# Optimization experiments

Hardware: AMD Instinct MI355X
Metric: run time of the kernel (lower is better)

Reference implementation:

```python
import jax, jax.numpy as jnp
import numpy as np
from jax import lax

C = 16
FIRE_RATE = 0.5
STEP_SIZE = 1.0


def _fixed_kernel():
    _i = np.array([0, 1, 0], dtype=np.float32)
    I = np.outer(_i, _i)
    dx = (np.outer([1, 2, 1], [-1, 0, 1]) / 8.0).astype(np.float32)
    dy = dx.T
    lap = np.array([[0.25, 0.5, 0.25], [0.5, -3, 0.5], [0.25, 0.5, 0.25]], dtype=np.float32)
    av = np.ones((3, 3), dtype=np.float32) / 9.0
    k = np.stack([I, dx, dy, lap, av], -1)            # [3,3,5]
    k = np.tile(k, (1, 1, C))                          # [3,3,5*C], channel-major blocks of 5
    return jnp.asarray(k[:, :, None, :])               # HWIO [3,3,1,5*C]

KERNEL = _fixed_kernel()


def setup_inputs() -> dict:
    key = jax.random.key(0)
    ks = jax.random.split(key, 5)
    B, S = 4, 512
    x = jax.random.normal(ks[0], (B, S, S, C), jnp.float32)
    noise = jax.random.normal(ks[1], (B, S, S, 1), jnp.float32)
    W1 = jax.random.normal(ks[2], (5 * C, 4 * C), jnp.float32) * (1.0 / np.sqrt(5 * C))
    b1 = jnp.zeros((4 * C,), jnp.float32)
    W2 = jax.random.normal(ks[3], (4 * C, 2 * C), jnp.float32) * (1.0 / np.sqrt(4 * C))
    b2 = jnp.zeros((2 * C,), jnp.float32)
    W3 = jax.random.normal(ks[4], (2 * C, C), jnp.float32) * (1.0 / np.sqrt(2 * C))
    b3 = jnp.zeros((C,), jnp.float32)
    return {"x": x, "noise": noise, "W1": W1, "b1": b1, "W2": W2, "b2": b2, "W3": W3, "b3": b3}


def _swish(z):
    return z * jax.nn.sigmoid(z)


def reference(x, noise, W1, b1, W2, b2, W3, b3):
    # perceive: depthwise 3x3 conv with 5 fixed kernels per channel -> [B,H,W,5*C]
    y = lax.conv_general_dilated(
        x, KERNEL, window_strides=(1, 1), padding="SAME",
        dimension_numbers=("NHWC", "HWIO", "NHWC"), feature_group_count=C)
    # 3-layer 1x1 conv MLP
    h = _swish(jnp.einsum("bhwc,cd->bhwd", y, W1) + b1)
    h = _swish(jnp.einsum("bhwc,cd->bhwd", h, W2) + b2)
    dx = (jnp.einsum("bhwc,cd->bhwd", h, W3) + b3) * STEP_SIZE
    # stochastic update mask: normal noise <= fire_rate
    update_mask = (noise <= FIRE_RATE).astype(jnp.float32)  # [B,H,W,1]
    return x + dx * update_mask
```

## Files before the change

### kernel.cpp

```cpp
#include <hip/hip_runtime.h>

typedef __bf16 bf16x8 __attribute__((ext_vector_type(8)));
typedef float f32x16 __attribute__((ext_vector_type(16)));
typedef short short8 __attribute__((ext_vector_type(8)));

#define S 512
#define CH 16

#define ELT(v, c) ((c)==0 ? (v).x : (c)==1 ? (v).y : (c)==2 ? (v).z : (v).w)

__device__ __forceinline__ float swishf(float z) {
    return z * __builtin_amdgcn_rcpf(1.0f + __expf(-z));
}

__global__ void prep_weights(const float* __restrict__ W1, const float* __restrict__ b1,
                             const float* __restrict__ W2, const float* __restrict__ b2,
                             const float* __restrict__ W3, const float* __restrict__ b3,
                             short* __restrict__ wsf, float* __restrict__ wsb)
{
    int idx = blockIdx.x * 256 + threadIdx.x;
    if (idx < 12288) {
        int fi = idx >> 9, rem = idx & 511;
        int lane = rem >> 3, j = rem & 7;
        int col = lane & 31, hi = lane >> 5;
        int jp = (j & 3) + 8 * (j >> 2);
        float v;
        if (fi < 18) {
            int n = fi / 9, s = fi - n * 9;
            int dr = s / 3, dc = s - dr * 3;
            int c = hi * 8 + j;
            const float wgt0 = (dr == 1) ? 2.f : 1.f;
            const float wgt1 = (dc == 1) ? 2.f : 1.f;
            const float dlt0 = (float)(dr - 1);
            const float dlt1 = (float)(dc - 1);
            const float lapm[9] = {0.25f, 0.5f, 0.25f, 0.5f, -3.f, 0.5f, 0.25f, 0.5f, 0.25f};
            float kI  = (s == 4) ? 1.f : 0.f;
            float kdx = wgt0 * dlt1 * 0.125f;
            float kdy = dlt0 * wgt1 * 0.125f;
            float klp = lapm[s];
            float kav = 1.f / 9.f;
            const float* wr = W1 + (c * 5) * 64 + n * 32 + col;
            v = kI * wr[0] + kdx * wr[64] + kdy * wr[128] + klp * wr[192] + kav * wr[256];
        } else if (fi < 22) {
            int t = fi - 18;
            int rowW = (t >> 1) * 32 + 4 * hi + (t & 1) * 16 + jp;
            v = W2[rowW * 32 + col];
        } else {
            int t = fi - 22;
            int rowW = 4 * hi + t * 16 + jp;
            v = (col < 16) ? W3[rowW * 16 + col] : 0.0f;
        }
        __bf16 b = (__bf16)v;
        wsf[idx] = __builtin_bit_cast(short, b);
    }
    if (blockIdx.x == 0) {
        int t = threadIdx.x;
        if (t < 64) wsb[t] = b1[t];
        else if (t < 96) wsb[t] = b2[t - 64];
        else if (t < 112) wsb[t] = b3[t - 96];
    }
}

__global__ __launch_bounds__(256, 4) void nca_fused(
    const float* __restrict__ x, const float* __restrict__ noise,
    const short* __restrict__ wsf, const float* __restrict__ wsb,
    float* __restrict__ out)
{
    __shared__ short wlds[12288];
    {
        const int4* src = reinterpret_cast<const int4*>(wsf);
        int4* dst = reinterpret_cast<int4*>(wlds);
        for (int i = threadIdx.x; i < 1536; i += 256) dst[i] = src[i];
    }
    __syncthreads();

    const int tid = threadIdx.x;
    const int bid = blockIdx.x;
    const int st = bid & 15;
    const int rg = (bid >> 4) & 127;
    const int bb = bid >> 11;
    const int wv = tid >> 6, lane = tid & 63;
    const int col = lane & 31, hi = lane >> 5;
    const int row = rg * 4 + wv;
    const int px0 = st * 32;

    short8 bfr[9];
    {
        const float* xb = x + (size_t)bb * S * S * CH + hi * 8;
        const bool rowInt = (row > 0) && (row < S - 1);
        const bool colInt = (px0 != 0) && (px0 != 480);
        if (rowInt && colInt) {
#pragma unroll
            for (int dr = 0; dr < 3; ++dr) {
                const float* rp = xb + ((size_t)(row - 1 + dr) * S + (px0 + col - 1)) * CH;
#pragma unroll
                for (int dc = 0; dc < 3; ++dc) {
                    float4 v0 = *reinterpret_cast<const float4*>(rp + dc * CH);
                    float4 v1 = *reinterpret_cast<const float4*>(rp + dc * CH + 4);
                    short8 f;
                    f[0] = __builtin_bit_cast(short, (__bf16)v0.x);
                    f[1] = __builtin_bit_cast(short, (__bf16)v0.y);
                    f[2] = __builtin_bit_cast(short, (__bf16)v0.z);
                    f[3] = __builtin_bit_cast(short, (__bf16)v0.w);
                    f[4] = __builtin_bit_cast(short, (__bf16)v1.x);
                    f[5] = __builtin_bit_cast(short, (__bf16)v1.y);
                    f[6] = __builtin_bit_cast(short, (__bf16)v1.z);
                    f[7] = __builtin_bit_cast(short, (__bf16)v1.w);
                    bfr[dr * 3 + dc] = f;
                }
            }
        } else {
#pragma unroll
            for (int dr = 0; dr < 3; ++dr) {
                int gr = row - 1 + dr;
                bool rok = (unsigned)gr < (unsigned)S;
                int grc = min(max(gr, 0), S - 1);
#pragma unroll
                for (int dc = 0; dc < 3; ++dc) {
                    int c = px0 + col - 1 + dc;
                    bool ok = rok && ((unsigned)c < (unsigned)S);
                    int cl = min(max(c, 0), S - 1);
                    const float* p = xb + ((size_t)grc * S + cl) * CH;
                    float4 v0 = *reinterpret_cast<const float4*>(p);
                    float4 v1 = *reinterpret_cast<const float4*>(p + 4);
                    if (!ok) { v0 = make_float4(0.f,0.f,0.f,0.f); v1 = v0; }
                    short8 f;
                    f[0] = __builtin_bit_cast(short, (__bf16)v0.x);
                    f[1] = __builtin_bit_cast(short, (__bf16)v0.y);
                    f[2] = __builtin_bit_cast(short, (__bf16)v0.z);
                    f[3] = __builtin_bit_cast(short, (__bf16)v0.w);
                    f[4] = __builtin_bit_cast(short, (__bf16)v1.x);
                    f[5] = __builtin_bit_cast(short, (__bf16)v1.y);
                    f[6] = __builtin_bit_cast(short, (__bf16)v1.z);
                    f[7] = __builtin_bit_cast(short, (__bf16)v1.w);
                    bfr[dr * 3 + dc] = f;
                }
            }
        }
    }

    const short8* wf = reinterpret_cast<const short8*>(wlds);

    f32x16 acc1[2];
#pragma unroll
    for (int n = 0; n < 2; ++n) {
        f32x16 acc = {};
#pragma unroll
        for (int s = 0; s < 9; ++s) {
            bf16x8 a = __builtin_bit_cast(bf16x8, wf[(n * 9 + s) * 64 + lane]);
            acc = __builtin_amdgcn_mfma_f32_32x32x16_bf16(a, __builtin_bit_cast(bf16x8, bfr[s]), acc, 0, 0, 0);
        }
        acc1[n] = acc;
    }

    short8 b2f[4];
#pragma unroll
    for (int t = 0; t < 4; ++t) {
        int n = t >> 1;
        float4 bq0 = *reinterpret_cast<const float4*>(wsb + n * 32 + 4 * hi + 16 * (t & 1));
        float4 bq1 = *reinterpret_cast<const float4*>(wsb + n * 32 + 4 * hi + 16 * (t & 1) + 8);
#pragma unroll
        for (int j = 0; j < 8; ++j) {
            float bias = (j < 4) ? ELT(bq0, j & 3) : ELT(bq1, j & 3);
            float h = swishf(acc1[n][(t & 1) * 8 + j] + bias);
            b2f[t][j] = __builtin_bit_cast(short, (__bf16)h);
        }
    }

    f32x16 acc2 = {};
#pragma unroll
    for (int t = 0; t < 4; ++t) {
        bf16x8 a = __builtin_bit_cast(bf16x8, wf[(18 + t) * 64 + lane]);
        acc2 = __builtin_amdgcn_mfma_f32_32x32x16_bf16(a, __builtin_bit_cast(bf16x8, b2f[t]), acc2, 0, 0, 0);
    }

    short8 b3f[2];
#pragma unroll
    for (int t = 0; t < 2; ++t) {
        float4 cq0 = *reinterpret_cast<const float4*>(wsb + 64 + 4 * hi + 16 * t);
        float4 cq1 = *reinterpret_cast<const float4*>(wsb + 64 + 4 * hi + 16 * t + 8);
#pragma unroll
        for (int j = 0; j < 8; ++j) {
            float bias = (j < 4) ? ELT(cq0, j & 3) : ELT(cq1, j & 3);
            float h = swishf(acc2[t * 8 + j] + bias);
            b3f[t][j] = __builtin_bit_cast(short, (__bf16)h);
        }
    }

    f32x16 acc3 = {};
#pragma unroll
    for (int t = 0; t < 2; ++t) {
        bf16x8 a = __builtin_bit_cast(bf16x8, wf[(22 + t) * 64 + lane]);
        acc3 = __builtin_amdgcn_mfma_f32_32x32x16_bf16(a, __builtin_bit_cast(bf16x8, b3f[t]), acc3, 0, 0, 0);
    }

    size_t pix = ((size_t)(bb * S + row)) * S + px0 + col;
    float msk = (noise[pix] <= 0.5f) ? 1.f : 0.f;
    float4 bA = *reinterpret_cast<const float4*>(wsb + 96 + 4 * hi);
    float4 bB = *reinterpret_cast<const float4*>(wsb + 96 + 8 + 4 * hi);
    const float* xp = x + pix * CH;
    float4 c0 = *reinterpret_cast<const float4*>(xp + 4 * hi);
    float4 c1 = *reinterpret_cast<const float4*>(xp + 8 + 4 * hi);
    float4 o0, o1;
    o0.x = c0.x + (acc3[0] + bA.x) * msk;
    o0.y = c0.y + (acc3[1] + bA.y) * msk;
    o0.z = c0.z + (acc3[2] + bA.z) * msk;
    o0.w = c0.w + (acc3[3] + bA.w) * msk;
    o1.x = c1.x + (acc3[4] + bB.x) * msk;
    o1.y = c1.y + (acc3[5] + bB.y) * msk;
    o1.z = c1.z + (acc3[6] + bB.z) * msk;
    o1.w = c1.w + (acc3[7] + bB.w) * msk;
    *reinterpret_cast<float4*>(out + pix * CH + 4 * hi) = o0;
    *reinterpret_cast<float4*>(out + pix * CH + 8 + 4 * hi) = o1;
}

extern "C" void kernel_launch(void* const* d_in, const int* in_sizes, int n_in,
                              void* d_out, int out_size, void* d_ws, size_t ws_size,
                              hipStream_t stream)
{
    const float* x     = (const float*)d_in[0];
    const float* noise = (const float*)d_in[1];
    const float* W1    = (const float*)d_in[2];
    const float* b1    = (const float*)d_in[3];
    const float* W2    = (const float*)d_in[4];
    const float* b2    = (const float*)d_in[5];
    const float* W3    = (const float*)d_in[6];
    const float* b3    = (const float*)d_in[7];
    short* wsf = (short*)d_ws;
    float* wsb = (float*)((char*)d_ws + 24576);
    float* out = (float*)d_out;

    hipLaunchKernelGGL(prep_weights, dim3(48), dim3(256), 0, stream,
                       W1, b1, W2, b2, W3, b3, wsf, wsb);
    hipLaunchKernelGGL(nca_fused, dim3(4 * 128 * 16), dim3(256), 0, stream,
                       x, noise, wsf, wsb, out);
}
```

Baseline: 180.1 us.

## Process eight rows per wave with a rolling three-row register window

Each wave now computes 8 consecutive output rows, keeping the converted bf16 stencil fragments for three input rows in registers and loading only one new row per step, which cuts redundant global loads and bf16 conversions of the 3x3 neighbourhood. The grid shrinks eightfold, so the weight copy into LDS is amortised over more pixels, and the next row's loads are issued before the MFMA chain to overlap memory with compute. The W3 column order is permuted so each lane writes 8 contiguous output channels as two float4 stores. Risks include higher register pressure (occupancy hint lowered to 3) and fewer blocks to hide latency.

New measurement: 208.0 us. +15.5%, slower.

```diff
diff --git a/kernel.cpp b/kernel.cpp
--- a/kernel.cpp
+++ b/kernel.cpp
@@ -48,7 +48,8 @@
         } else {
             int t = fi - 22;
             int rowW = 4 * hi + t * 16 + jp;
-            v = (col < 16) ? W3[rowW * 16 + col] : 0.0f;
+            int ch = (col & 3) | (((col >> 3) & 1) << 2) | (((col >> 2) & 1) << 3);
+            v = (col < 16) ? W3[rowW * 16 + ch] : 0.0f;
         }
         __bf16 b = (__bf16)v;
         wsf[idx] = __builtin_bit_cast(short, b);
@@ -61,7 +62,56 @@
     }
 }
 
-__global__ __launch_bounds__(256, 4) void nca_fused(
+__device__ __forceinline__ void loadrow(const float* __restrict__ xb, int gr, int px0,
+                                        int col, int hi, bool edgeStrip, float4 L[3][2])
+{
+    const bool rv = (unsigned)gr < (unsigned)S;
+    const int grc = rv ? gr : (gr < 0 ? 0 : S - 1);
+    if (!edgeStrip) {
+        const float* rp = xb + ((size_t)grc * S + (px0 + col - 1)) * CH + hi * 8;
+#pragma unroll
+        for (int dc = 0; dc < 3; ++dc) {
+            L[dc][0] = *reinterpret_cast<const float4*>(rp + dc * CH);
+            L[dc][1] = *reinterpret_cast<const float4*>(rp + dc * CH + 4);
+        }
+    } else {
+#pragma unroll
+        for (int dc = 0; dc < 3; ++dc) {
+            int c = px0 + col - 1 + dc;
+            bool ok = (unsigned)c < (unsigned)S;
+            int cl = min(max(c, 0), S - 1);
+            const float* p = xb + ((size_t)grc * S + cl) * CH + hi * 8;
+            float4 v0 = *reinterpret_cast<const float4*>(p);
+            float4 v1 = *reinterpret_cast<const float4*>(p + 4);
+            if (!ok) { v0 = make_float4(0.f, 0.f, 0.f, 0.f); v1 = v0; }
+            L[dc][0] = v0; L[dc][1] = v1;
+        }
+    }
+    if (!rv) {
+#pragma unroll
+        for (int dc = 0; dc < 3; ++dc) {
+            L[dc][0] = make_float4(0.f, 0.f, 0.f, 0.f);
+            L[dc][1] = L[dc][0];
+        }
+    }
+}
+
+__device__ __forceinline__ short8 cvt2(float4 a, float4 b) {
+    short8 f;
+    f[0] = __builtin_bit_cast(short, (__bf16)a.x);
+    f[1] = __builtin_bit_cast(short, (__bf16)a.y);
+    f[2] = __builtin_bit_cast(short, (__bf16)a.z);
+    f[3] = __builtin_bit_cast(short, (__bf16)a.w);
+    f[4] = __builtin_bit_cast(short, (__bf16)b.x);
+    f[5] = __builtin_bit_cast(short, (__bf16)b.y);
+    f[6] = __builtin_bit_cast(short, (__bf16)b.z);
+    f[7] = __builtin_bit_cast(short, (__bf16)b.w);
+    return f;
+}
+
+#define NR 8
+
+__global__ __launch_bounds__(256, 3) void nca_fused(
     const float* __restrict__ x, const float* __restrict__ noise,
     const short* __restrict__ wsf, const float* __restrict__ wsb,
     float* __restrict__ out)
@@ -74,144 +124,122 @@
     }
     __syncthreads();
 
-    const int tid = threadIdx.x;
-    const int bid = blockIdx.x;
-    const int st = bid & 15;
-    const int rg = (bid >> 4) & 127;
-    const int bb = bid >> 11;
+    const int tid = threadIdx.x, bid = blockIdx.x;
     const int wv = tid >> 6, lane = tid & 63;
     const int col = lane & 31, hi = lane >> 5;
-    const int row = rg * 4 + wv;
+    const int st = bid & 15;
+    const int rgp = (bid >> 4) & 15;
+    const int bb = bid >> 8;
     const int px0 = st * 32;
-
-    short8 bfr[9];
+    const int r0 = (rgp * 4 + wv) * NR;
+    const bool edgeStrip = (px0 == 0) || (px0 == 480);
+    const float* xb = x + (size_t)bb * S * S * CH;
+    const short8* wf = reinterpret_cast<const short8*>(wlds);
+
+    float4 bA = *reinterpret_cast<const float4*>(wsb + 96 + 8 * hi);
+    float4 bB = *reinterpret_cast<const float4*>(wsb + 96 + 8 * hi + 4);
+
+    short8 fr[3][3];
     {
-        const float* xb = x + (size_t)bb * S * S * CH + hi * 8;
-        const bool rowInt = (row > 0) && (row < S - 1);
-        const bool colInt = (px0 != 0) && (px0 != 480);
-        if (rowInt && colInt) {
-#pragma unroll
-            for (int dr = 0; dr < 3; ++dr) {
-                const float* rp = xb + ((size_t)(row - 1 + dr) * S + (px0 + col - 1)) * CH;
-#pragma unroll
-                for (int dc = 0; dc < 3; ++dc) {
-                    float4 v0 = *reinterpret_cast<const float4*>(rp + dc * CH);
-                    float4 v1 = *reinterpret_cast<const float4*>(rp + dc * CH + 4);
-                    short8 f;
-                    f[0] = __builtin_bit_cast(short, (__bf16)v0.x);
-                    f[1] = __builtin_bit_cast(short, (__bf16)v0.y);
-                    f[2] = __builtin_bit_cast(short, (__bf16)v0.z);
-                    f[3] = __builtin_bit_cast(short, (__bf16)v0.w);
-                    f[4] = __builtin_bit_cast(short, (__bf16)v1.x);
-                    f[5] = __builtin_bit_cast(short, (__bf16)v1.y);
-                    f[6] = __builtin_bit_cast(short, (__bf16)v1.z);
-                    f[7] = __builtin_bit_cast(short, (__bf16)v1.w);
-                    bfr[dr * 3 + dc] = f;
-                }
+        float4 P[3][2];
+        loadrow(xb, r0 - 1, px0, col, hi, edgeStrip, P);
+#pragma unroll
+        for (int dc = 0; dc < 3; ++dc) fr[0][dc] = cvt2(P[dc][0], P[dc][1]);
+        loadrow(xb, r0, px0, col, hi, edgeStrip, P);
+#pragma unroll
+        for (int dc = 0; dc < 3; ++dc) fr[1][dc] = cvt2(P[dc][0], P[dc][1]);
+        loadrow(xb, r0 + 1, px0, col, hi, edgeStrip, P);
+#pragma unroll
+        for (int dc = 0; dc < 3; ++dc) fr[2][dc] = cvt2(P[dc][0], P[dc][1]);
+    }
+
+#pragma unroll
+    for (int i = 0; i < NR; ++i) {
+        const int r = r0 + i;
+
+        float4 NL[3][2];
+        loadrow(xb, r + 2, px0, col, hi, edgeStrip, NL);
+
+        const float* cp = xb + ((size_t)r * S + px0 + col) * CH + 8 * hi;
+        float4 c0 = *reinterpret_cast<const float4*>(cp);
+        float4 c1 = *reinterpret_cast<const float4*>(cp + 4);
+        float nz = noise[((size_t)(bb * S + r)) * S + px0 + col];
+
+        f32x16 acc1[2] = {{}, {}};
+#pragma unroll
+        for (int dr = 0; dr < 3; ++dr)
+#pragma unroll
+            for (int dc = 0; dc < 3; ++dc) {
+                const int s = dr * 3 + dc;
+                bf16x8 bfrag = __builtin_bit_cast(bf16x8, fr[(i + dr) % 3][dc]);
+                bf16x8 a0 = __builtin_bit_cast(bf16x8, wf[s * 64 + lane]);
+                bf16x8 a1 = __builtin_bit_cast(bf16x8, wf[(9 + s) * 64 + lane]);
+                acc1[0] = __builtin_amdgcn_mfma_f32_32x32x16_bf16(a0, bfrag, acc1[0], 0, 0, 0);
+                acc1[1] = __builtin_amdgcn_mfma_f32_32x32x16_bf16(a1, bfrag, acc1[1], 0, 0, 0);
             }
-        } else {
-#pragma unroll
-            for (int dr = 0; dr < 3; ++dr) {
-                int gr = row - 1 + dr;
-                bool rok = (unsigned)gr < (unsigned)S;
-                int grc = min(max(gr, 0), S - 1);
-#pragma unroll
-                for (int dc = 0; dc < 3; ++dc) {
-                    int c = px0 + col - 1 + dc;
-                    bool ok = rok && ((unsigned)c < (unsigned)S);
-                    int cl = min(max(c, 0), S - 1);
-                    const float* p = xb + ((size_t)grc * S + cl) * CH;
-                    float4 v0 = *reinterpret_cast<const float4*>(p);
-                    float4 v1 = *reinterpret_cast<const float4*>(p + 4);
-                    if (!ok) { v0 = make_float4(0.f,0.f,0.f,0.f); v1 = v0; }
-                    short8 f;
-                    f[0] = __builtin_bit_cast(short, (__bf16)v0.x);
-                    f[1] = __builtin_bit_cast(short, (__bf16)v0.y);
-                    f[2] = __builtin_bit_cast(short, (__bf16)v0.z);
-                    f[3] = __builtin_bit_cast(short, (__bf16)v0.w);
-                    f[4] = __builtin_bit_cast(short, (__bf16)v1.x);
-                    f[5] = __builtin_bit_cast(short, (__bf16)v1.y);
-                    f[6] = __builtin_bit_cast(short, (__bf16)v1.z);
-                    f[7] = __builtin_bit_cast(short, (__bf16)v1.w);
-                    bfr[dr * 3 + dc] = f;
-                }
+
+        short8 b2f[4];
+#pragma unroll
+        for (int t = 0; t < 4; ++t) {
+            int n = t >> 1;
+            float4 bq0 = *reinterpret_cast<const float4*>(wsb + n * 32 + 4 * hi + 16 * (t & 1));
+            float4 bq1 = *reinterpret_cast<const float4*>(wsb + n * 32 + 4 * hi + 16 * (t & 1) + 8);
+#pragma unroll
+            for (int j = 0; j < 8; ++j) {
+                float bias = (j < 4) ? ELT(bq0, j & 3) : ELT(bq1, j & 3);
+                float h = swishf(acc1[n][(t & 1) * 8 + j] + bias);
+                b2f[t][j] = __builtin_bit_cast(short, (__bf16)h);
             }
         }
-    }
-
-    const short8* wf = reinterpret_cast<const short8*>(wlds);
-
-    f32x16 acc1[2];
-#pragma unroll
-    for (int n = 0; n < 2; ++n) {
-        f32x16 acc = {};
-#pragma unroll
-        for (int s = 0; s < 9; ++s) {
-            bf16x8 a = __builtin_bit_cast(bf16x8, wf[(n * 9 + s) * 64 + lane]);
-            acc = __builtin_amdgcn_mfma_f32_32x32x16_bf16(a, __builtin_bit_cast(bf16x8, bfr[s]), acc, 0, 0, 0);
-        }
-        acc1[n] = acc;
-    }
-
-    short8 b2f[4];
-#pragma unroll
-    for (int t = 0; t < 4; ++t) {
-        int n = t >> 1;
-        float4 bq0 = *reinterpret_cast<const float4*>(wsb + n * 32 + 4 * hi + 16 * (t & 1));
-        float4 bq1 = *reinterpret_cast<const float4*>(wsb + n * 32 + 4 * hi + 16 * (t & 1) + 8);
-#pragma unroll
-        for (int j = 0; j < 8; ++j) {
-            float bias = (j < 4) ? ELT(bq0, j & 3) : ELT(bq1, j & 3);
-            float h = swishf(acc1[n][(t & 1) * 8 + j] + bias);
-            b2f[t][j] = __builtin_bit_cast(short, (__bf16)h);
-        }
-    }
-
-    f32x16 acc2 = {};
-#pragma unroll
-    for (int t = 0; t < 4; ++t) {
-        bf16x8 a = __builtin_bit_cast(bf16x8, wf[(18 + t) * 64 + lane]);
-        acc2 = __builtin_amdgcn_mfma_f32_32x32x16_bf16(a, __builtin_bit_cast(bf16x8, b2f[t]), acc2, 0, 0, 0);
-    }
-
-    short8 b3f[2];
-#pragma unroll
-    for (int t = 0; t < 2; ++t) {
-        float4 cq0 = *reinterpret_cast<const float4*>(wsb + 64 + 4 * hi + 16 * t);
-        float4 cq1 = *reinterpret_cast<const float4*>(wsb + 64 + 4 * hi + 16 * t + 8);
-#pragma unroll
-        for (int j = 0; j < 8; ++j) {
-            float bias = (j < 4) ? ELT(cq0, j & 3) : ELT(cq1, j & 3);
-            float h = swishf(acc2[t * 8 + j] + bias);
-            b3f[t][j] = __builtin_bit_cast(short, (__bf16)h);
-        }
-    }
-
-    f32x16 acc3 = {};
-#pragma unroll
-    for (int t = 0; t < 2; ++t) {
-        bf16x8 a = __builtin_bit_cast(bf16x8, wf[(22 + t) * 64 + lane]);
-        acc3 = __builtin_amdgcn_mfma_f32_32x32x16_bf16(a, __builtin_bit_cast(bf16x8, b3f[t]), acc3, 0, 0, 0);
-    }
-
-    size_t pix = ((size_t)(bb * S + row)) * S + px0 + col;
-    float msk = (noise[pix] <= 0.5f) ? 1.f : 0.f;
-    float4 bA = *reinterpret_cast<const float4*>(wsb + 96 + 4 * hi);
-    float4 bB = *reinterpret_cast<const float4*>(wsb + 96 + 8 + 4 * hi);
-    const float* xp = x + pix * CH;
-    float4 c0 = *reinterpret_cast<const float4*>(xp + 4 * hi);
-    float4 c1 = *reinterpret_cast<const float4*>(xp + 8 + 4 * hi);
-    float4 o0, o1;
-    o0.x = c0.x + (acc3[0] + bA.x) * msk;
-    o0.y = c0.y + (acc3[1] + bA.y) * msk;
-    o0.z = c0.z + (acc3[2] + bA.z) * msk;
-    o0.w = c0.w + (acc3[3] + bA.w) * msk;
-    o1.x = c1.x + (acc3[4] + bB.x) * msk;
-    o1.y = c1.y + (acc3[5] + bB.y) * msk;
-    o1.z = c1.z + (acc3[6] + bB.z) * msk;
-    o1.w = c1.w + (acc3[7] + bB.w) * msk;
-    *reinterpret_cast<float4*>(out + pix * CH + 4 * hi) = o0;
-    *reinterpret_cast<float4*>(out + pix * CH + 8 + 4 * hi) = o1;
+
+        f32x16 acc2 = {};
+#pragma unroll
+        for (int t = 0; t < 4; ++t) {
+            bf16x8 a = __builtin_bit_cast(bf16x8, wf[(18 + t) * 64 + lane]);
+            acc2 = __builtin_amdgcn_mfma_f32_32x32x16_bf16(a, __builtin_bit_cast(bf16x8, b2f[t]), acc2, 0, 0, 0);
+        }
+
+        short8 b3f[2];
+#pragma unroll
+        for (int t = 0; t < 2; ++t) {
+            float4 cq0 = *reinterpret_cast<const float4*>(wsb + 64 + 4 * hi + 16 * t);
+            float4 cq1 = *reinterpret_cast<const float4*>(wsb + 64 + 4 * hi + 16 * t + 8);
+#pragma unroll
+            for (int j = 0; j < 8; ++j) {
+                float bias = (j < 4) ? ELT(cq0, j & 3) : ELT(cq1, j & 3);
+                float h = swishf(acc2[t * 8 + j] + bias);
+                b3f[t][j] = __builtin_bit_cast(short, (__bf16)h);
+            }
+        }
+
+        f32x16 acc3 = {};
+#pragma unroll
+        for (int t = 0; t < 2; ++t) {
+            bf16x8 a = __builtin_bit_cast(bf16x8, wf[(22 + t) * 64 + lane]);
+            acc3 = __builtin_amdgcn_mfma_f32_32x32x16_bf16(a, __builtin_bit_cast(bf16x8, b3f[t]), acc3, 0, 0, 0);
+        }
+
+        {
+            size_t pix = ((size_t)(bb * S + r)) * S + px0 + col;
+            float msk = (nz <= 0.5f) ? 1.f : 0.f;
+            float4 o0, o1;
+            o0.x = c0.x + (acc3[0] + bA.x) * msk;
+            o0.y = c0.y + (acc3[1] + bA.y) * msk;
+            o0.z = c0.z + (acc3[2] + bA.z) * msk;
+            o0.w = c0.w + (acc3[3] + bA.w) * msk;
+            o1.x = c1.x + (acc3[4] + bB.x) * msk;
+            o1.y = c1.y + (acc3[5] + bB.y) * msk;
+            o1.z = c1.z + (acc3[6] + bB.z) * msk;
+            o1.w = c1.w + (acc3[7] + bB.w) * msk;
+            float* op = out + pix * CH + 8 * hi;
+            *reinterpret_cast<float4*>(op) = o0;
+            *reinterpret_cast<float4*>(op + 4) = o1;
+        }
+
+#pragma unroll
+        for (int dc = 0; dc < 3; ++dc)
+            fr[i % 3][dc] = cvt2(NL[dc][0], NL[dc][1]);
+    }
 }
 
 extern "C" void kernel_launch(void* const* d_in, const int* in_sizes, int n_in,
@@ -232,6 +260,6 @@
 
     hipLaunchKernelGGL(prep_weights, dim3(48), dim3(256), 0, stream,
                        W1, b1, W2, b2, W3, b3, wsf, wsb);
-    hipLaunchKernelGGL(nca_fused, dim3(4 * 128 * 16), dim3(256), 0, stream,
+    hipLaunchKernelGGL(nca_fused, dim3(4 * 16 * 16), dim3(256), 0, stream,
                        x, noise, wsf, wsb, out);
 }
```
